# Optimization experiments

Hardware: AMD Instinct MI355X
Metric: run time of the kernel (lower is better)

The kernel has to match this reference:

```python
import jax, jax.numpy as jnp
import numpy as np

B, T, DIM = 2, 2048, 1024
H, HD = 16, 64          # num_heads, head_dim (DIM = H*HD)
SCALE = 0.12            # fixed attn_scale in the module
ROPE_BASE = 1024.0
EPS = 1e-6


def _rope_tables(seq_len, head_dim):
    half = head_dim // 2
    keep = head_dim // 4
    active = (1.0 / ROPE_BASE) ** jnp.linspace(0.0, 1.0, keep, dtype=jnp.float32)
    inv_freq = jnp.concatenate([active, jnp.zeros(half - keep, dtype=jnp.float32)])
    theta = jnp.arange(seq_len, dtype=jnp.float32)[:, None] * inv_freq[None, :]  # [T, half]
    return jnp.cos(theta), jnp.sin(theta)


def _rms_norm(x):
    # F.rms_norm without learned scale
    return x * jax.lax.rsqrt(jnp.mean(x * x, axis=-1, keepdims=True) + EPS)


def _apply_rope(x_bthd, cos, sin):
    # x_bthd: [B,T,H,HD]; cos/sin: [T, HD/2]
    xf = x_bthd.astype(jnp.float32)
    x1, x2 = jnp.split(xf, 2, axis=-1)
    c = cos[None, :, None, :]
    s = sin[None, :, None, :]
    y = jnp.concatenate([x1 * c + x2 * s, -x1 * s + x2 * c], axis=-1)
    return y.astype(x_bthd.dtype)


def setup_inputs() -> dict:
    key = jax.random.key(0)
    k1, k2, k3, k4 = jax.random.split(key, 4)
    x = jax.random.normal(k1, (B, T, DIM), dtype=jnp.float32)
    ve = jax.random.normal(k2, (B, T, DIM), dtype=jnp.float32)
    sa_lambdas = jax.random.uniform(k3, (2,), dtype=jnp.float32)
    # additive causal mask, as SDPA receives a float mask cast to q dtype
    causal = jnp.tril(jnp.ones((T, T), dtype=bool))
    attn_mask = jnp.where(causal, 0.0, -1e9).astype(jnp.float32)[None, None]
    # qkvo weights; scaled like a typical linear init (original zero-inits W_o,
    # here kept random so the output is non-trivial for kernel testing)
    qkvo_w = jax.random.normal(k4, (4, DIM, DIM), dtype=jnp.float32) * (DIM ** -0.5)
    return {"x": x, "ve": ve, "sa_lambdas": sa_lambdas, "attn_mask": attn_mask, "qkvo_w": qkvo_w}


def reference(x, ve, sa_lambdas, attn_mask, qkvo_w):
    b, t, _ = x.shape
    # fused QKV projection: qkvo_w[:3] is [3, DIM, DIM], F.linear -> x @ W.T
    qkv = jnp.einsum('btd,ked->btke', x, qkvo_w[:3])          # [B,T,3,DIM]
    q = _rms_norm(qkv[:, :, 0].reshape(b, t, H, HD))
    k = _rms_norm(qkv[:, :, 1].reshape(b, t, H, HD))
    v = _rms_norm(qkv[:, :, 2].reshape(b, t, H, HD))
    cos, sin = _rope_tables(t, HD)
    q = _apply_rope(q, cos, sin)
    k = _apply_rope(k, cos, sin)
    # value-embedding blend
    v = sa_lambdas[0] * v + sa_lambdas[1] * ve.reshape(b, t, H, HD)
    # attention with fixed scale and additive mask
    scores = jnp.einsum('bthd,bshd->bhts', q, k) * SCALE + attn_mask
    att = jax.nn.softmax(scores, axis=-1)
    y = jnp.einsum('bhts,bshd->bthd', att, v).reshape(b, t, DIM)
    return y @ qkvo_w[3].T
```

## Files before the change

kernel.cpp:

```cpp
#include <hip/hip_runtime.h>
#include <hip/hip_bf16.h>
#include <stdint.h>

#define T_SEQ 2048
#define DIMSZ 1024
#define NH    16
#define HDIM  64
#define NBATCH 2
#define KVB   64
#define ATT_SCALE 0.12f
#define QSCALE (0.12f * 1.4426950408889634f)

typedef __attribute__((ext_vector_type(8))) __bf16 bf16x8;
typedef __attribute__((ext_vector_type(8))) ushort u16x8;
typedef __attribute__((ext_vector_type(4))) float f32x4;

#define GLOAD_LDS16(gp, lp)                                                            \
  __builtin_amdgcn_global_load_lds((const __attribute__((address_space(1))) void*)(gp),\
                                   (__attribute__((address_space(3))) void*)(lp),      \
                                   16, 0, 0)

__device__ __forceinline__ ushort f2bf(float f) {
  union { float f; uint32_t u; } v; v.f = f;
  uint32_t u = v.u;
  uint32_t r = (u + 0x7FFFu + ((u >> 16) & 1u)) >> 16;
  return (ushort)r;
}

__device__ __forceinline__ float bf2f(ushort h) {
  union { float f; uint32_t u; } v;
  v.u = ((uint32_t)h) << 16;
  return v.f;
}

__device__ __forceinline__ uint32_t pk2(float a, float b) {
  union { __hip_bfloat162 h; uint32_t u; } cv;
  cv.h = __hip_bfloat162(__float2bfloat16(a), __float2bfloat16(b));
  return cv.u;
}

__global__ __launch_bounds__(256) void conv_bf16_k(const float* __restrict__ in,
                                                   ushort* __restrict__ out, int n) {
  int i = (blockIdx.x * 256 + threadIdx.x) * 4;
  if (i >= n) return;
  float4 v = *(const float4*)(in + i);
  ushort4 o;
  o.x = f2bf(v.x); o.y = f2bf(v.y); o.z = f2bf(v.z); o.w = f2bf(v.w);
  *(ushort4*)(out + i) = o;
}

__global__ __launch_bounds__(256) void rope_tab_k(float* __restrict__ ctab,
                                                  float* __restrict__ stab) {
  int idx = blockIdx.x * 256 + threadIdx.x;
  if (idx >= T_SEQ * 32) return;
  int j = idx & 31, t = idx >> 5;
  float c = 1.f, s = 0.f;
  if (j < 16) {
    float inv = powf(1024.0f, -(float)j / 15.0f);
    float th = (float)t * inv;
    c = cosf(th);
    s = sinf(th);
  }
  ctab[idx] = c;
  stab[idx] = s;
}

#define BM 128
#define BN 128
#define BKS 64

__global__ __launch_bounds__(256) void gemm_out_k(const ushort* __restrict__ A,
                                                  const ushort* __restrict__ Bt,
                                                  float* __restrict__ C) {
  const int K = DIMSZ, N = DIMSZ;
  __shared__ __align__(16) ushort As[64 * BKS];
  __shared__ __align__(16) ushort Bs[128 * BKS];
  int tid = threadIdx.x;
  int wave = tid >> 6, lane = tid & 63;
  int lr = lane & 15, lg = lane >> 4;
  int m0 = blockIdx.x * 64, n0 = blockIdx.y * 128;
  int wm = (wave >> 1) * 32, wn = (wave & 1) * 64;

  int srow = tid >> 3;
  int sel = (((tid & 7) ^ (srow & 7)) << 3);

  f32x4 acc[2][4];
#pragma unroll
  for (int m = 0; m < 2; ++m)
#pragma unroll
    for (int n = 0; n < 4; ++n)
      acc[m][n] = (f32x4){0.f, 0.f, 0.f, 0.f};

  for (int k0 = 0; k0 < K; k0 += BKS) {
#pragma unroll
    for (int it = 0; it < 2; ++it)
      GLOAD_LDS16(A + (size_t)(m0 + it * 32 + srow) * K + k0 + sel, &As[(it * 256 + tid) * 8]);
#pragma unroll
    for (int it = 0; it < 4; ++it)
      GLOAD_LDS16(Bt + (size_t)(n0 + it * 32 + srow) * K + k0 + sel, &Bs[(it * 256 + tid) * 8]);
    __syncthreads();
#pragma unroll
    for (int kk = 0; kk < 2; ++kk) {
      int cA = (((kk * 4 + lg) ^ (lr & 7)) << 3);
      bf16x8 af[2], bf[4];
#pragma unroll
      for (int m = 0; m < 2; ++m)
        af[m] = *(const bf16x8*)&As[(wm + m * 16 + lr) * BKS + cA];
#pragma unroll
      for (int n = 0; n < 4; ++n)
        bf[n] = *(const bf16x8*)&Bs[(wn + n * 16 + lr) * BKS + cA];
#pragma unroll
      for (int m = 0; m < 2; ++m)
#pragma unroll
        for (int n = 0; n < 4; ++n)
          acc[m][n] = __builtin_amdgcn_mfma_f32_16x16x32_bf16(af[m], bf[n], acc[m][n], 0, 0, 0);
    }
    __syncthreads();
  }
#pragma unroll
  for (int m = 0; m < 2; ++m)
#pragma unroll
    for (int n = 0; n < 4; ++n)
#pragma unroll
      for (int r = 0; r < 4; ++r) {
        int row = m0 + wm + m * 16 + lg * 4 + r;
        int col = n0 + wn + n * 16 + lr;
        C[(size_t)row * N + col] = acc[m][n][r];
      }
}

__global__ __launch_bounds__(256) void gemm_qkv_k(const ushort* __restrict__ A,
                                                  const ushort* __restrict__ Bt,
                                                  const float* __restrict__ ve,
                                                  const float* __restrict__ lam,
                                                  const float* __restrict__ ctab,
                                                  const float* __restrict__ stab,
                                                  ushort* __restrict__ Qb,
                                                  ushort* __restrict__ Kb,
                                                  ushort* __restrict__ Vt) {
  const int K = DIMSZ;
  __shared__ __align__(16) ushort As[BM * BKS];
  __shared__ __align__(16) ushort Bs[BN * BKS];
  int tid = threadIdx.x;
  int wave = tid >> 6, lane = tid & 63;
  int lr = lane & 15, lg = lane >> 4;
  int m0 = blockIdx.x * BM, n0 = blockIdx.y * BN;
  int wm = (wave >> 1) * 64, wn = (wave & 1) * 64;

  int srow = tid >> 3;
  int sel = (((tid & 7) ^ (srow & 7)) << 3);

  f32x4 acc[4][4];
  for (int m = 0; m < 4; ++m)
    for (int n = 0; n < 4; ++n)
      acc[m][n] = (f32x4){0.f, 0.f, 0.f, 0.f};

  for (int k0 = 0; k0 < K; k0 += BKS) {
#pragma unroll
    for (int it = 0; it < 4; ++it) {
      GLOAD_LDS16(A + (size_t)(m0 + it * 32 + srow) * K + k0 + sel, &As[(it * 256 + tid) * 8]);
      GLOAD_LDS16(Bt + (size_t)(n0 + it * 32 + srow) * K + k0 + sel, &Bs[(it * 256 + tid) * 8]);
    }
    __syncthreads();
#pragma unroll
    for (int kk = 0; kk < 2; ++kk) {
      int cA = (((kk * 4 + lg) ^ (lr & 7)) << 3);
      bf16x8 af[4], bf[4];
#pragma unroll
      for (int m = 0; m < 4; ++m)
        af[m] = *(const bf16x8*)&As[(wm + m * 16 + lr) * BKS + cA];
#pragma unroll
      for (int n = 0; n < 4; ++n)
        bf[n] = *(const bf16x8*)&Bs[(wn + n * 16 + lr) * BKS + cA];
#pragma unroll
      for (int m = 0; m < 4; ++m)
#pragma unroll
        for (int n = 0; n < 4; ++n)
          acc[m][n] = __builtin_amdgcn_mfma_f32_16x16x32_bf16(af[m], bf[n], acc[m][n], 0, 0, 0);
    }
    __syncthreads();
  }

  int sec = n0 >> 10;
  int h = ((n0 & 1023) + wn) >> 6;
  ushort* Tl = (wave < 2 ? As : Bs) + (wave & 1) * 4096;

#pragma unroll
  for (int m = 0; m < 4; ++m)
#pragma unroll
    for (int n = 0; n < 4; ++n)
#pragma unroll
      for (int r = 0; r < 4; ++r) {
        int tl = m * 16 + lg * 4 + r;
        int d = n * 16 + lr;
        Tl[tl * 64 + ((((d >> 3) ^ (tl & 7)) << 3) | (d & 7))] = f2bf(acc[m][n][r]);
      }

  int tl = lane;
  float xv[64];
#pragma unroll
  for (int j = 0; j < 8; ++j) {
    u16x8 rw = *(const u16x8*)&Tl[tl * 64 + ((j ^ (tl & 7)) << 3)];
#pragma unroll
    for (int e = 0; e < 8; ++e) xv[j * 8 + e] = bf2f((ushort)rw[e]);
  }

  float ss = 0.f;
#pragma unroll
  for (int i = 0; i < 64; ++i) ss += xv[i] * xv[i];
  float rinv = rsqrtf(ss * (1.0f / 64.0f) + 1e-6f);
#pragma unroll
  for (int i = 0; i < 64; ++i) xv[i] *= rinv;

  int row = m0 + wm + tl;
  int t = row & (T_SEQ - 1);
  int bb = row >> 11;
  int bh = bb * NH + h;

  if (sec < 2) {
    float cs[16], sn[16];
    const float4* cp = (const float4*)(ctab + t * 32);
    const float4* sp = (const float4*)(stab + t * 32);
#pragma unroll
    for (int j = 0; j < 4; ++j) {
      float4 c4 = cp[j], s4 = sp[j];
      cs[j * 4 + 0] = c4.x; cs[j * 4 + 1] = c4.y; cs[j * 4 + 2] = c4.z; cs[j * 4 + 3] = c4.w;
      sn[j * 4 + 0] = s4.x; sn[j * 4 + 1] = s4.y; sn[j * 4 + 2] = s4.z; sn[j * 4 + 3] = s4.w;
    }
#pragma unroll
    for (int j = 0; j < 16; ++j) {
      float a = xv[j], bv = xv[j + 32];
      xv[j] = a * cs[j] + bv * sn[j];
      xv[j + 32] = bv * cs[j] - a * sn[j];
    }
    float sc = (sec == 0) ? QSCALE : 1.0f;
    ushort* dst = (sec == 0 ? Qb : Kb) + ((size_t)bh * T_SEQ + t) * HDIM;
#pragma unroll
    for (int p = 0; p < 8; ++p) {
      uint4 wq = make_uint4(pk2(xv[8 * p] * sc, xv[8 * p + 1] * sc),
                            pk2(xv[8 * p + 2] * sc, xv[8 * p + 3] * sc),
                            pk2(xv[8 * p + 4] * sc, xv[8 * p + 5] * sc),
                            pk2(xv[8 * p + 6] * sc, xv[8 * p + 7] * sc));
      *((uint4*)dst + p) = wq;
    }
  } else {
    float l0 = lam[0], l1 = lam[1];
    const float4* vp = (const float4*)(ve + ((size_t)(bb * T_SEQ + t)) * DIMSZ + h * HDIM);
#pragma unroll
    for (int j = 0; j < 16; ++j) {
      float4 vv4 = vp[j];
      xv[j * 4 + 0] = l0 * xv[j * 4 + 0] + l1 * vv4.x;
      xv[j * 4 + 1] = l0 * xv[j * 4 + 1] + l1 * vv4.y;
      xv[j * 4 + 2] = l0 * xv[j * 4 + 2] + l1 * vv4.z;
      xv[j * 4 + 3] = l0 * xv[j * 4 + 3] + l1 * vv4.w;
    }
    ushort* dst = Vt + (size_t)bh * HDIM * T_SEQ + t;
#pragma unroll
    for (int i = 0; i < 64; ++i)
      dst[(size_t)i * T_SEQ] = f2bf(xv[i]);
  }
}

__global__ __launch_bounds__(512, 4) void attn_k(const ushort* __restrict__ Q,
                                                 const ushort* __restrict__ K,
                                                 const ushort* __restrict__ Vt,
                                                 ushort* __restrict__ Y) {
  int bh = blockIdx.x;
  int pair = blockIdx.y;
  int tid = threadIdx.x;
  int wid = tid >> 6, lane = tid & 63;
  int lr = lane & 15, lg = lane >> 4;
  int b = bh >> 4, h = bh & 15;

  int NT = 32 - pair;
  int grp = wid >> 2;
  int myqb = grp ? (31 - pair) : pair;
  int mylast = grp ? (NT - 1) : pair;
  int strip = wid & 3;
  int r0 = myqb * 64 + strip * 16;

  __shared__ __align__(16) ushort Kl[2][KVB * HDIM];
  __shared__ __align__(16) ushort Vl[2][KVB * HDIM];
  __shared__ __align__(16) ushort Plds[8][16][72];

  const ushort* Kbh = K + (size_t)bh * T_SEQ * HDIM;
  const ushort* Vbh = Vt + (size_t)bh * HDIM * T_SEQ;

  int srow = tid >> 3, schunk = tid & 7;
  int sel = ((schunk ^ (srow & 7)) << 3);
  const ushort* ksrc = Kbh + (size_t)srow * HDIM + sel;
  const ushort* vsrc = Vbh + (size_t)srow * T_SEQ + sel;
  int ldst = wid << 9;

  const ushort* Qbase = Q + ((size_t)bh * T_SEQ + r0) * HDIM;
  bf16x8 aq[2];
#pragma unroll
  for (int kk = 0; kk < 2; ++kk)
    aq[kk] = *(const bf16x8*)(Qbase + (size_t)lr * HDIM + kk * 32 + lg * 8);

  int fcol[2];
  fcol[0] = ((0 + lg) ^ (lr & 7)) << 3;
  fcol[1] = ((4 + lg) ^ (lr & 7)) << 3;

  f32x4 o[4];
#pragma unroll
  for (int n = 0; n < 4; ++n) o[n] = (f32x4){0.f, 0.f, 0.f, 0.f};
  float lrow = 0.f;

  GLOAD_LDS16(ksrc, &Kl[0][ldst]);
  GLOAD_LDS16(vsrc, &Vl[0][ldst]);
  __syncthreads();

  int cur = 0;
  for (int kb = 0; kb < NT; ++kb) {
    if (kb + 1 < NT) {
      GLOAD_LDS16(ksrc + (size_t)(kb + 1) * KVB * HDIM, &Kl[cur ^ 1][ldst]);
      GLOAD_LDS16(vsrc + (kb + 1) * KVB, &Vl[cur ^ 1][ldst]);
    }
    if (kb <= mylast) {
      const ushort* Kc = &Kl[cur][0];
      const ushort* Vc = &Vl[cur][0];
      f32x4 s[4];
#pragma unroll
      for (int n = 0; n < 4; ++n) {
        f32x4 a = (f32x4){0.f, 0.f, 0.f, 0.f};
        bf16x8 kf0 = *(const bf16x8*)&Kc[(n * 16 + lr) * HDIM + fcol[0]];
        a = __builtin_amdgcn_mfma_f32_16x16x32_bf16(kf0, aq[0], a, 0, 0, 0);
        bf16x8 kf1 = *(const bf16x8*)&Kc[(n * 16 + lr) * HDIM + fcol[1]];
        a = __builtin_amdgcn_mfma_f32_16x16x32_bf16(kf1, aq[1], a, 0, 0, 0);
        s[n] = a;
      }
      if (kb == mylast) {
        int qrow = r0 + lr;
        int kb0 = kb * KVB + lg * 4;
#pragma unroll
        for (int n = 0; n < 4; ++n)
#pragma unroll
          for (int r = 0; r < 4; ++r)
            if (kb0 + n * 16 + r > qrow) s[n][r] = -1e30f;
      }
      float psum = 0.f;
#pragma unroll
      for (int n = 0; n < 4; ++n) {
        float p0 = exp2f(s[n][0]), p1 = exp2f(s[n][1]);
        float p2 = exp2f(s[n][2]), p3 = exp2f(s[n][3]);
        psum += (p0 + p1) + (p2 + p3);
        uint2 w;
        w.x = pk2(p0, p1);
        w.y = pk2(p2, p3);
        *(uint2*)&Plds[wid][lr][n * 16 + lg * 4] = w;
      }
      lrow += psum;
#pragma unroll
      for (int kk = 0; kk < 2; ++kk) {
        bf16x8 ap = *(const bf16x8*)&Plds[wid][lr][kk * 32 + lg * 8];
#pragma unroll
        for (int n = 0; n < 4; ++n) {
          bf16x8 vf = *(const bf16x8*)&Vc[(n * 16 + lr) * HDIM + fcol[kk]];
          o[n] = __builtin_amdgcn_mfma_f32_16x16x32_bf16(vf, ap, o[n], 0, 0, 0);
        }
      }
    }
    __syncthreads();
    cur ^= 1;
  }
  lrow += __shfl_xor(lrow, 16);
  lrow += __shfl_xor(lrow, 32);
  float inv = 1.0f / lrow;
  int row = r0 + lr;
#pragma unroll
  for (int n = 0; n < 4; ++n) {
    uint2 w;
    w.x = pk2(o[n][0] * inv, o[n][1] * inv);
    w.y = pk2(o[n][2] * inv, o[n][3] * inv);
    *(uint2*)&Y[((size_t)b * T_SEQ + row) * DIMSZ + h * HDIM + n * 16 + lg * 4] = w;
  }
}

extern "C" void kernel_launch(void* const* d_in, const int* in_sizes, int n_in,
                              void* d_out, int out_size, void* d_ws, size_t ws_size,
                              hipStream_t stream) {
  const float* x   = (const float*)d_in[0];
  const float* ve  = (const float*)d_in[1];
  const float* lam = (const float*)d_in[2];
  const float* w   = (const float*)d_in[4];
  float* out = (float*)d_out;

  char* ws = (char*)d_ws;
  const size_t NTOK = (size_t)NBATCH * T_SEQ;
  const size_t nX = NTOK * DIMSZ;
  const size_t nW = 4ull * DIMSZ * DIMSZ;

  ushort* Xb   = (ushort*)(ws);
  ushort* Wb   = (ushort*)(ws + 8388608);
  ushort* Qb   = (ushort*)(ws + 16777216);
  ushort* Kb   = (ushort*)(ws + 25165824);
  ushort* Vt   = (ushort*)(ws + 33554432);
  ushort* Yb   = (ushort*)(ws + 41943040);
  float*  ctab = (float*)(ws + 50331648);
  float*  stab = (float*)(ws + 50593792);

  conv_bf16_k<<<(int)(nX / 4 / 256), 256, 0, stream>>>(x, Xb, (int)nX);
  conv_bf16_k<<<(int)(nW / 4 / 256), 256, 0, stream>>>(w, Wb, (int)nW);
  rope_tab_k<<<(T_SEQ * 32) / 256, 256, 0, stream>>>(ctab, stab);

  gemm_qkv_k<<<dim3(4096 / BM, 3072 / BN), 256, 0, stream>>>(Xb, Wb, ve, lam, ctab, stab,
                                                             Qb, Kb, Vt);

  attn_k<<<dim3(NBATCH * NH, 16), 512, 0, stream>>>(Qb, Kb, Vt, Yb);

  gemm_out_k<<<dim3(4096 / 64, 1024 / 128), 256, 0, stream>>>(Yb, Wb + 3ull * DIMSZ * DIMSZ, out);
}
```

Baseline: 125.0 us.

## Replace paired causal query blocks with one query block per workgroup

Instead of one 512-thread workgroup holding two query blocks (pair and 31-pair) that share K/V tiles for load balance, each 256-thread workgroup now handles a single 64-row query block, launched heaviest-first (qb = 31 - blockIdx.y). The grid doubles, the per-iteration idle-wave check goes away, and each thread issues two async loads per tile. The cost is that K/V tiles are no longer shared between the paired blocks, so global/L2 traffic for K/V roughly doubles, and balance now depends on the hardware scheduler.

```diff
diff --git a/kernel.cpp b/kernel.cpp
--- a/kernel.cpp
+++ b/kernel.cpp
@@ -261,36 +261,34 @@
   }
 }
 
-__global__ __launch_bounds__(512, 4) void attn_k(const ushort* __restrict__ Q,
+__global__ __launch_bounds__(256, 3) void attn_k(const ushort* __restrict__ Q,
                                                  const ushort* __restrict__ K,
                                                  const ushort* __restrict__ Vt,
                                                  ushort* __restrict__ Y) {
   int bh = blockIdx.x;
-  int pair = blockIdx.y;
+  int qb = 31 - blockIdx.y;
   int tid = threadIdx.x;
   int wid = tid >> 6, lane = tid & 63;
   int lr = lane & 15, lg = lane >> 4;
   int b = bh >> 4, h = bh & 15;
 
-  int NT = 32 - pair;
-  int grp = wid >> 2;
-  int myqb = grp ? (31 - pair) : pair;
-  int mylast = grp ? (NT - 1) : pair;
-  int strip = wid & 3;
-  int r0 = myqb * 64 + strip * 16;
+  int r0 = qb * 64 + wid * 16;
+  int nkv = qb + 1;
 
   __shared__ __align__(16) ushort Kl[2][KVB * HDIM];
   __shared__ __align__(16) ushort Vl[2][KVB * HDIM];
-  __shared__ __align__(16) ushort Plds[8][16][72];
+  __shared__ __align__(16) ushort Plds[4][16][72];
 
   const ushort* Kbh = K + (size_t)bh * T_SEQ * HDIM;
   const ushort* Vbh = Vt + (size_t)bh * HDIM * T_SEQ;
 
-  int srow = tid >> 3, schunk = tid & 7;
-  int sel = ((schunk ^ (srow & 7)) << 3);
-  const ushort* ksrc = Kbh + (size_t)srow * HDIM + sel;
-  const ushort* vsrc = Vbh + (size_t)srow * T_SEQ + sel;
-  int ldst = wid << 9;
+  int sr = tid >> 3;
+  int sel = (((tid & 7) ^ (sr & 7)) << 3);
+  const ushort* ksrc0 = Kbh + (size_t)sr * HDIM + sel;
+  const ushort* ksrc1 = Kbh + (size_t)(sr + 32) * HDIM + sel;
+  const ushort* vsrc0 = Vbh + (size_t)sr * T_SEQ + sel;
+  const ushort* vsrc1 = Vbh + (size_t)(sr + 32) * T_SEQ + sel;
+  int ld0 = tid * 8, ld1 = tid * 8 + 2048;
 
   const ushort* Qbase = Q + ((size_t)bh * T_SEQ + r0) * HDIM;
   bf16x8 aq[2];
@@ -307,62 +305,65 @@
   for (int n = 0; n < 4; ++n) o[n] = (f32x4){0.f, 0.f, 0.f, 0.f};
   float lrow = 0.f;
 
-  GLOAD_LDS16(ksrc, &Kl[0][ldst]);
-  GLOAD_LDS16(vsrc, &Vl[0][ldst]);
+  GLOAD_LDS16(ksrc0, &Kl[0][ld0]);
+  GLOAD_LDS16(ksrc1, &Kl[0][ld1]);
+  GLOAD_LDS16(vsrc0, &Vl[0][ld0]);
+  GLOAD_LDS16(vsrc1, &Vl[0][ld1]);
   __syncthreads();
 
-  int cur = 0;
-  for (int kb = 0; kb < NT; ++kb) {
-    if (kb + 1 < NT) {
-      GLOAD_LDS16(ksrc + (size_t)(kb + 1) * KVB * HDIM, &Kl[cur ^ 1][ldst]);
-      GLOAD_LDS16(vsrc + (kb + 1) * KVB, &Vl[cur ^ 1][ldst]);
-    }
-    if (kb <= mylast) {
-      const ushort* Kc = &Kl[cur][0];
-      const ushort* Vc = &Vl[cur][0];
-      f32x4 s[4];
+  for (int kb = 0; kb < nkv; ++kb) {
+    int cur = kb & 1;
+    if (kb + 1 < nkv) {
+      size_t ko = (size_t)(kb + 1) * KVB * HDIM;
+      int vo = (kb + 1) * KVB;
+      GLOAD_LDS16(ksrc0 + ko, &Kl[cur ^ 1][ld0]);
+      GLOAD_LDS16(ksrc1 + ko, &Kl[cur ^ 1][ld1]);
+      GLOAD_LDS16(vsrc0 + vo, &Vl[cur ^ 1][ld0]);
+      GLOAD_LDS16(vsrc1 + vo, &Vl[cur ^ 1][ld1]);
+    }
+    const ushort* Kc = &Kl[cur][0];
+    const ushort* Vc = &Vl[cur][0];
+    f32x4 s[4];
+#pragma unroll
+    for (int n = 0; n < 4; ++n) {
+      f32x4 a = (f32x4){0.f, 0.f, 0.f, 0.f};
+      bf16x8 kf0 = *(const bf16x8*)&Kc[(n * 16 + lr) * HDIM + fcol[0]];
+      a = __builtin_amdgcn_mfma_f32_16x16x32_bf16(kf0, aq[0], a, 0, 0, 0);
+      bf16x8 kf1 = *(const bf16x8*)&Kc[(n * 16 + lr) * HDIM + fcol[1]];
+      a = __builtin_amdgcn_mfma_f32_16x16x32_bf16(kf1, aq[1], a, 0, 0, 0);
+      s[n] = a;
+    }
+    if (kb == nkv - 1) {
+      int qrow = r0 + lr;
+      int kb0 = kb * KVB + lg * 4;
+#pragma unroll
+      for (int n = 0; n < 4; ++n)
+#pragma unroll
+        for (int r = 0; r < 4; ++r)
+          if (kb0 + n * 16 + r > qrow) s[n][r] = -1e30f;
+    }
+    float psum = 0.f;
+#pragma unroll
+    for (int n = 0; n < 4; ++n) {
+      float p0 = exp2f(s[n][0]), p1 = exp2f(s[n][1]);
+      float p2 = exp2f(s[n][2]), p3 = exp2f(s[n][3]);
+      psum += (p0 + p1) + (p2 + p3);
+      uint2 w;
+      w.x = pk2(p0, p1);
+      w.y = pk2(p2, p3);
+      *(uint2*)&Plds[wid][lr][n * 16 + lg * 4] = w;
+    }
+    lrow += psum;
+#pragma unroll
+    for (int kk = 0; kk < 2; ++kk) {
+      bf16x8 ap = *(const bf16x8*)&Plds[wid][lr][kk * 32 + lg * 8];
 #pragma unroll
       for (int n = 0; n < 4; ++n) {
-        f32x4 a = (f32x4){0.f, 0.f, 0.f, 0.f};
-        bf16x8 kf0 = *(const bf16x8*)&Kc[(n * 16 + lr) * HDIM + fcol[0]];
-        a = __builtin_amdgcn_mfma_f32_16x16x32_bf16(kf0, aq[0], a, 0, 0, 0);
-        bf16x8 kf1 = *(const bf16x8*)&Kc[(n * 16 + lr) * HDIM + fcol[1]];
-        a = __builtin_amdgcn_mfma_f32_16x16x32_bf16(kf1, aq[1], a, 0, 0, 0);
-        s[n] = a;
+        bf16x8 vf = *(const bf16x8*)&Vc[(n * 16 + lr) * HDIM + fcol[kk]];
+        o[n] = __builtin_amdgcn_mfma_f32_16x16x32_bf16(vf, ap, o[n], 0, 0, 0);
       }
-      if (kb == mylast) {
-        int qrow = r0 + lr;
-        int kb0 = kb * KVB + lg * 4;
-#pragma unroll
-        for (int n = 0; n < 4; ++n)
-#pragma unroll
-          for (int r = 0; r < 4; ++r)
-            if (kb0 + n * 16 + r > qrow) s[n][r] = -1e30f;
-      }
-      float psum = 0.f;
-#pragma unroll
-      for (int n = 0; n < 4; ++n) {
-        float p0 = exp2f(s[n][0]), p1 = exp2f(s[n][1]);
-        float p2 = exp2f(s[n][2]), p3 = exp2f(s[n][3]);
-        psum += (p0 + p1) + (p2 + p3);
-        uint2 w;
-        w.x = pk2(p0, p1);
-        w.y = pk2(p2, p3);
-        *(uint2*)&Plds[wid][lr][n * 16 + lg * 4] = w;
-      }
-      lrow += psum;
-#pragma unroll
-      for (int kk = 0; kk < 2; ++kk) {
-        bf16x8 ap = *(const bf16x8*)&Plds[wid][lr][kk * 32 + lg * 8];
-#pragma unroll
-        for (int n = 0; n < 4; ++n) {
-          bf16x8 vf = *(const bf16x8*)&Vc[(n * 16 + lr) * HDIM + fcol[kk]];
-          o[n] = __builtin_amdgcn_mfma_f32_16x16x32_bf16(vf, ap, o[n], 0, 0, 0);
-        }
-      }
     }
     __syncthreads();
-    cur ^= 1;
   }
   lrow += __shfl_xor(lrow, 16);
   lrow += __shfl_xor(lrow, 32);
@@ -407,7 +408,7 @@
   gemm_qkv_k<<<dim3(4096 / BM, 3072 / BN), 256, 0, stream>>>(Xb, Wb, ve, lam, ctab, stab,
                                                              Qb, Kb, Vt);
 
-  attn_k<<<dim3(NBATCH * NH, 16), 512, 0, stream>>>(Qb, Kb, Vt, Yb);
+  attn_k<<<dim3(NBATCH * NH, 32), 256, 0, stream>>>(Qb, Kb, Vt, Yb);
 
   gemm_out_k<<<dim3(4096 / 64, 1024 / 128), 256, 0, stream>>>(Yb, Wb + 3ull * DIMSZ * DIMSZ, out);
 }
```

New measurement: 120.9 us. 3.3% less time.
